# Performance work log

Hardware: AMD Instinct MI355X
Metric: run time of the kernel (lower is better)

The kernel has to match this reference:

```python
import jax, jax.numpy as jnp
import numpy as np

PAD = 4
MAX_DISP = 4


def setup_inputs() -> dict:
    key = jax.random.key(0)
    k1, k2 = jax.random.split(key)
    in1 = jax.random.normal(k1, (8, 256, 128, 128), dtype=jnp.float32)
    in2 = jax.random.normal(k2, (8, 256, 128, 128), dtype=jnp.float32)
    return {"in1": in1, "in2": in2}


def reference(in1, in2):
    # in1, in2: [B, C, H, W]
    H, W = in1.shape[2], in1.shape[3]
    in2_pad = jnp.pad(in2, ((0, 0), (0, 0), (PAD, PAD), (PAD, PAD)))
    D = 2 * MAX_DISP + 1  # 9 displacements per axis -> 81 output channels
    outs = []
    # torch.meshgrid('ij') + zip(offsetx, offsety): dy is the outer (slow) index,
    # dx the inner (fast) index.
    for dy in range(D):
        for dx in range(D):
            # mean over channel dim of elementwise product with shifted window
            corr = jnp.mean(in1 * in2_pad[:, :, dy:dy + H, dx:dx + W],
                            axis=1, keepdims=True)  # [B,1,H,W]
            outs.append(corr)
    return jnp.concatenate(outs, axis=1)  # [B, D*D, H, W]
```

## Files before the change

kernel.cpp:

```cpp
#include <hip/hip_runtime.h>
#include <stdint.h>


#define B_  8
#define C_  256
#define H_  128
#define W_  128
#define ND  9
#define TY  8
#define TW  16
#define KC  32
#define KB  4
#define RR  16
#define JJ  24
#define NITEM 3
#define NDMA  6
#define CS   (H_ * W_)
#define NCH  (C_ / KC)
#define SBUF (KC * RR * JJ)
#define FBUF (KB * RR * JJ * 8)
#define FOFF (2 * SBUF * 4)
#define LDS_TOTAL (FOFF + 2 * FBUF * 2)

typedef short v8s __attribute__((ext_vector_type(8)));
typedef float v4f __attribute__((ext_vector_type(4)));

__device__ __forceinline__ unsigned short f2bf(float f) {
    union { float f; unsigned u; } v; v.f = f;
    return (unsigned short)((v.u + 0x7FFFu + ((v.u >> 16) & 1u)) >> 16);
}

__device__ __forceinline__ void dma16(const float* g, void* lds) {
    __builtin_amdgcn_global_load_lds(
        (const __attribute__((address_space(1))) void*)g,
        (__attribute__((address_space(3))) void*)lds, 16, 0, 0);
}

#define FENCE()        asm volatile("" ::: "memory")
#define WAITV14_BAR()  asm volatile("s_waitcnt vmcnt(14)\n\ts_barrier" ::: "memory")
#define WAITV0_BAR()   asm volatile("s_waitcnt vmcnt(0)\n\ts_barrier" ::: "memory")
#define LGKM0_BAR()    asm volatile("s_waitcnt lgkmcnt(0)\n\ts_barrier" ::: "memory")
#define LGKM0()        asm volatile("s_waitcnt lgkmcnt(0)" ::: "memory")

__global__ __launch_bounds__(512, 2)
void corr_mfma_kernel(const float* __restrict__ in1,
                      const float* __restrict__ in2,
                      float* __restrict__ out) {
    extern __shared__ __align__(16) char ldsbase[];
    float* S = (float*)ldsbase;
    short* F = (short*)(ldsbase + FOFF);

    const int tid  = threadIdx.x;
    const int lane = tid & 63;
    const int w    = tid >> 6;

    const int lin = blockIdx.x;
    const int b   = lin & 7;
    const int idx = lin >> 3;
    const int by  = idx & 15;
    const int bx  = idx >> 4;
    const int x0  = bx * TW;
    const int y0  = by * TY;

    const int i_px = lane & 15;
    const int kb   = lane >> 4;

    const float* dsrc[NDMA];
    int ddst[NDMA];
    #pragma unroll
    for (int t = 0; t < NDMA; ++t) {
        const int q  = w * NDMA + t;
        const int g  = q * 64 + lane;
        const int cc = g / 96;
        const int rm = g % 96;
        const int r  = rm / 6;
        const int jg = rm % 6;
        int gy = y0 - 4 + r;
        int gx = x0 - 4 + jg * 4;
        gy = gy < 0 ? 0 : (gy > H_ - 1 ? H_ - 1 : gy);
        gx = gx < 0 ? 0 : (gx > W_ - 4 ? W_ - 4 : gx);
        dsrc[t] = in2 + ((long)(b * C_ + cc) * H_ + gy) * W_ + gx;
        ddst[t] = q * 1024;
    }

    int soff[NITEM], foff[NITEM];
    bool valid[NITEM];
    #pragma unroll
    for (int it = 0; it < NITEM; ++it) {
        const int s   = tid + it * 512;
        const int ikb = s / (RR * JJ);
        const int ir  = (s / JJ) % RR;
        const int ij  = s % JJ;
        soff[it]  = ikb * 8 * (RR * JJ) + ir * JJ + ij;
        foff[it]  = s * 8;
        valid[it] = ((unsigned)(y0 - 4 + ir) < (unsigned)H_) &&
                    ((unsigned)(x0 - 4 + ij) < (unsigned)W_);
    }

    const float* p1 =
        in1 + (((long)b * C_ + kb * 8) * H_ + (y0 + w)) * W_ + x0 + i_px;

    v4f acc0[ND];
    v4f acc1[5];
    #pragma unroll
    for (int d = 0; d < ND; ++d) acc0[d] = (v4f)0.0f;
    #pragma unroll
    for (int p = 0; p < 5; ++p)  acc1[p] = (v4f)0.0f;

    float a_buf[2][8];
    v8s afrag, afrag_nxt;

    #pragma unroll
    for (int t = 0; t < NDMA; ++t) dma16(dsrc[t], (char*)S + ddst[t]);
    #pragma unroll
    for (int e = 0; e < 8; ++e) a_buf[0][e] = p1[(long)e * CS];
    FENCE();
    #pragma unroll
    for (int t = 0; t < NDMA; ++t)
        dma16(dsrc[t] + (long)KC * CS, (char*)S + SBUF * 4 + ddst[t]);
    #pragma unroll
    for (int e = 0; e < 8; ++e) a_buf[1][e] = p1[(long)KC * CS + (long)e * CS];
    FENCE();
    WAITV14_BAR();
    #pragma unroll
    for (int e = 0; e < 8; ++e) afrag[e] = (short)f2bf(a_buf[0][e]);
    {
        v8s pk[NITEM];
        #pragma unroll
        for (int it = 0; it < NITEM; ++it) {
            #pragma unroll
            for (int e = 0; e < 8; ++e)
                pk[it][e] = (short)f2bf(S[soff[it] + e * (RR * JJ)]);
            if (!valid[it]) pk[it] = (v8s)0;
        }
        #pragma unroll
        for (int it = 0; it < NITEM; ++it)
            *(v8s*)&F[foff[it]] = pk[it];
    }
    LGKM0_BAR();

    #pragma unroll
    for (int k = 0; k < NCH; ++k) {
        const int cb = k & 1;

        if (k + 2 < NCH) {
            const long co = (long)(k + 2) * KC * CS;
            #pragma unroll
            for (int t = 0; t < NDMA; ++t)
                dma16(dsrc[t] + co, (char*)S + cb * (SBUF * 4) + ddst[t]);
            #pragma unroll
            for (int e = 0; e < 8; ++e) a_buf[cb][e] = p1[co + (long)e * CS];
            FENCE();
        }

        #pragma unroll
        for (int dy = 0; dy < ND; ++dy) {
            const int r = w + dy;
            const v8s bf = *(const v8s*)&F[cb * FBUF + ((kb * RR + r) * JJ + i_px) * 8];
            acc0[dy] = __builtin_amdgcn_mfma_f32_16x16x32_bf16(afrag, bf, acc0[dy], 0, 0, 0);
        }
        #pragma unroll
        for (int P = 0; P < 5; ++P) {
            int r = w + 2 * P + (i_px >> 3);
            if (r > RR - 1) r = RR - 1;
            const int j = 16 + (i_px & 7);
            const v8s bf = *(const v8s*)&F[cb * FBUF + ((kb * RR + r) * JJ + j) * 8];
            acc1[P] = __builtin_amdgcn_mfma_f32_16x16x32_bf16(afrag, bf, acc1[P], 0, 0, 0);
        }

        if (k + 1 < NCH) {
            if (k + 2 < NCH) { WAITV14_BAR(); } else { WAITV0_BAR(); }

            #pragma unroll
            for (int e = 0; e < 8; ++e) afrag_nxt[e] = (short)f2bf(a_buf[cb ^ 1][e]);
            v8s pk[NITEM];
            #pragma unroll
            for (int it = 0; it < NITEM; ++it) {
                #pragma unroll
                for (int e = 0; e < 8; ++e)
                    pk[it][e] = (short)f2bf(S[(cb ^ 1) * SBUF + soff[it] + e * (RR * JJ)]);
                if (!valid[it]) pk[it] = (v8s)0;
            }
            #pragma unroll
            for (int it = 0; it < NITEM; ++it)
                *(v8s*)&F[(cb ^ 1) * FBUF + foff[it]] = pk[it];
            afrag = afrag_nxt;

            LGKM0_BAR();
        }
    }

    LGKM0_BAR();
    float* epw = (float*)F + w * (16 * 24);
    const int g = lane >> 4;

    for (int dy = 0; dy < ND; ++dy) {
        #pragma unroll
        for (int q = 0; q < 4; ++q)
            epw[(g * 4 + q) * 24 + i_px] = acc0[dy][q];
        if ((i_px >> 3) == (dy & 1)) {
            #pragma unroll
            for (int q = 0; q < 4; ++q)
                epw[(g * 4 + q) * 24 + 16 + (i_px & 7)] = acc1[dy >> 1][q];
        }
        LGKM0();
        #pragma unroll
        for (int rep = 0; rep < 3; ++rep) {
            const int dx = g + rep * 4;
            if (dx < 9) {
                const float v = epw[i_px * 24 + i_px + dx] * (1.0f / 256.0f);
                out[((((long)b * 81) + dy * 9 + dx) * H_ + (y0 + w)) * W_ + x0 + i_px] = v;
            }
        }
        LGKM0();
    }
}

extern "C" void kernel_launch(void* const* d_in, const int* in_sizes, int n_in,
                              void* d_out, int out_size, void* d_ws, size_t ws_size,
                              hipStream_t stream) {
    const float* in1 = (const float*)d_in[0];
    const float* in2 = (const float*)d_in[1];
    float* outp      = (float*)d_out;
    (void)hipFuncSetAttribute((const void*)corr_mfma_kernel,
                              hipFuncAttributeMaxDynamicSharedMemorySize,
                              LDS_TOTAL);
    corr_mfma_kernel<<<1024, 512, LDS_TOTAL, stream>>>(in1, in2, outp);
}
```

Baseline: 96.02 us.

## Make blocks persistent over four row tiles with cross-tile prefetch

Each block now walks four vertically stacked 8-row tiles instead of one, and the grid shrinks from 1024 to 256 blocks. The first channel chunks of the next tile are prefetched during the last chunks of the current tile, so the pipeline fill and drain is paid once per block rather than once per tile. The epilogue moves to a separate LDS region so it does not conflict with the prefetched buffers. The cost is fewer blocks (256 across the CUs, so less occupancy and parallelism) and more LDS per block.

```diff
diff --git a/kernel.cpp b/kernel.cpp
--- a/kernel.cpp
+++ b/kernel.cpp
@@ -9,6 +9,7 @@
 #define ND  9
 #define TY  8
 #define TW  16
+#define NT  4
 #define KC  32
 #define KB  4
 #define RR  16
@@ -16,11 +17,12 @@
 #define NITEM 3
 #define NDMA  6
 #define CS   (H_ * W_)
-#define NCH  (C_ / KC)
+#define NCH  8
 #define SBUF (KC * RR * JJ)
 #define FBUF (KB * RR * JJ * 8)
 #define FOFF (2 * SBUF * 4)
-#define LDS_TOTAL (FOFF + 2 * FBUF * 2)
+#define EPOFF (FOFF + 2 * FBUF * 2)
+#define LDS_TOTAL (EPOFF + 8 * 16 * JJ * 4)
 
 typedef short v8s __attribute__((ext_vector_type(8)));
 typedef float v4f __attribute__((ext_vector_type(4)));
@@ -47,8 +49,9 @@
                       const float* __restrict__ in2,
                       float* __restrict__ out) {
     extern __shared__ __align__(16) char ldsbase[];
-    float* S = (float*)ldsbase;
-    short* F = (short*)(ldsbase + FOFF);
+    float* S  = (float*)ldsbase;
+    short* F  = (short*)(ldsbase + FOFF);
+    float* EP = (float*)(ldsbase + EPOFF);
 
     const int tid  = threadIdx.x;
     const int lane = tid & 63;
@@ -57,16 +60,14 @@
     const int lin = blockIdx.x;
     const int b   = lin & 7;
     const int idx = lin >> 3;
-    const int by  = idx & 15;
-    const int bx  = idx >> 4;
-    const int x0  = bx * TW;
-    const int y0  = by * TY;
+    const int x0  = (idx & 7) * TW;
+    int y0        = (idx >> 3) * (NT * TY);
 
     const int i_px = lane & 15;
     const int kb   = lane >> 4;
 
-    const float* dsrc[NDMA];
-    int ddst[NDMA];
+    const float* dbase[NDMA];
+    int drr[NDMA], ddst[NDMA];
     #pragma unroll
     for (int t = 0; t < NDMA; ++t) {
         const int q  = w * NDMA + t;
@@ -75,16 +76,22 @@
         const int rm = g % 96;
         const int r  = rm / 6;
         const int jg = rm % 6;
-        int gy = y0 - 4 + r;
         int gx = x0 - 4 + jg * 4;
+        gx = gx < 0 ? 0 : (gx > W_ - 4 ? W_ - 4 : gx);
+        dbase[t] = in2 + (long)(b * C_ + cc) * CS + gx;
+        drr[t]   = r;
+        ddst[t]  = q * 1024;
+    }
+    const float* dsrc[NDMA];
+    #pragma unroll
+    for (int t = 0; t < NDMA; ++t) {
+        int gy = y0 - 4 + drr[t];
         gy = gy < 0 ? 0 : (gy > H_ - 1 ? H_ - 1 : gy);
-        gx = gx < 0 ? 0 : (gx > W_ - 4 ? W_ - 4 : gx);
-        dsrc[t] = in2 + ((long)(b * C_ + cc) * H_ + gy) * W_ + gx;
-        ddst[t] = q * 1024;
-    }
-
-    int soff[NITEM], foff[NITEM];
-    bool valid[NITEM];
+        dsrc[t] = dbase[t] + (long)gy * W_;
+    }
+
+    int soff[NITEM], foff2[NITEM], irr[NITEM];
+    bool vx[NITEM];
     #pragma unroll
     for (int it = 0; it < NITEM; ++it) {
         const int s   = tid + it * 512;
@@ -92,21 +99,16 @@
         const int ir  = (s / JJ) % RR;
         const int ij  = s % JJ;
         soff[it]  = ikb * 8 * (RR * JJ) + ir * JJ + ij;
-        foff[it]  = s * 8;
-        valid[it] = ((unsigned)(y0 - 4 + ir) < (unsigned)H_) &&
-                    ((unsigned)(x0 - 4 + ij) < (unsigned)W_);
+        foff2[it] = s * 8;
+        irr[it]   = ir;
+        vx[it]    = (unsigned)(x0 - 4 + ij) < (unsigned)W_;
     }
 
     const float* p1 =
-        in1 + (((long)b * C_ + kb * 8) * H_ + (y0 + w)) * W_ + x0 + i_px;
+        in1 + ((long)b * C_ + kb * 8) * CS + (long)(y0 + w) * W_ + x0 + i_px;
 
     v4f acc0[ND];
     v4f acc1[5];
-    #pragma unroll
-    for (int d = 0; d < ND; ++d) acc0[d] = (v4f)0.0f;
-    #pragma unroll
-    for (int p = 0; p < 5; ++p)  acc1[p] = (v4f)0.0f;
-
     float a_buf[2][8];
     v8s afrag, afrag_nxt;
 
@@ -125,94 +127,126 @@
     #pragma unroll
     for (int e = 0; e < 8; ++e) afrag[e] = (short)f2bf(a_buf[0][e]);
     {
+        const int y04 = y0 - 4;
         v8s pk[NITEM];
         #pragma unroll
         for (int it = 0; it < NITEM; ++it) {
             #pragma unroll
             for (int e = 0; e < 8; ++e)
                 pk[it][e] = (short)f2bf(S[soff[it] + e * (RR * JJ)]);
-            if (!valid[it]) pk[it] = (v8s)0;
+            if (!(vx[it] && (unsigned)(y04 + irr[it]) < (unsigned)H_)) pk[it] = (v8s)0;
         }
         #pragma unroll
         for (int it = 0; it < NITEM; ++it)
-            *(v8s*)&F[foff[it]] = pk[it];
+            *(v8s*)&F[foff2[it]] = pk[it];
     }
     LGKM0_BAR();
 
-    #pragma unroll
-    for (int k = 0; k < NCH; ++k) {
-        const int cb = k & 1;
-
-        if (k + 2 < NCH) {
-            const long co = (long)(k + 2) * KC * CS;
+    #pragma unroll 1
+    for (int tt = 0; tt < NT; ++tt) {
+        #pragma unroll
+        for (int d = 0; d < ND; ++d) acc0[d] = (v4f)0.0f;
+        #pragma unroll
+        for (int p = 0; p < 5; ++p)  acc1[p] = (v4f)0.0f;
+
+        #pragma unroll
+        for (int k = 0; k < NCH; ++k) {
+            const int cb = k & 1;
+            const bool last_tile  = (tt == NT - 1);
+            const bool has_issue  = (k < 6) || !last_tile;
+            const bool last_chunk = last_tile && (k == 7);
+
+            if (k == 6 && !last_tile) {
+                #pragma unroll
+                for (int t = 0; t < NDMA; ++t) {
+                    int gy = y0 + TY - 4 + drr[t];
+                    gy = gy < 0 ? 0 : (gy > H_ - 1 ? H_ - 1 : gy);
+                    dsrc[t] = dbase[t] + (long)gy * W_;
+                }
+            }
+            if (k < 6) {
+                const long co = (long)(k + 2) * KC * CS;
+                #pragma unroll
+                for (int t = 0; t < NDMA; ++t)
+                    dma16(dsrc[t] + co, (char*)S + cb * (SBUF * 4) + ddst[t]);
+                #pragma unroll
+                for (int e = 0; e < 8; ++e) a_buf[cb][e] = p1[co + (long)e * CS];
+                FENCE();
+            } else if (!last_tile) {
+                const long co = (long)(k - 6) * KC * CS;
+                const float* p1n = p1 + TY * W_;
+                #pragma unroll
+                for (int t = 0; t < NDMA; ++t)
+                    dma16(dsrc[t] + co, (char*)S + cb * (SBUF * 4) + ddst[t]);
+                #pragma unroll
+                for (int e = 0; e < 8; ++e) a_buf[cb][e] = p1n[co + (long)e * CS];
+                FENCE();
+            }
+
             #pragma unroll
-            for (int t = 0; t < NDMA; ++t)
-                dma16(dsrc[t] + co, (char*)S + cb * (SBUF * 4) + ddst[t]);
+            for (int dy = 0; dy < ND; ++dy) {
+                const int r = w + dy;
+                const v8s bf = *(const v8s*)&F[cb * FBUF + ((kb * RR + r) * JJ + i_px) * 8];
+                acc0[dy] = __builtin_amdgcn_mfma_f32_16x16x32_bf16(afrag, bf, acc0[dy], 0, 0, 0);
+            }
             #pragma unroll
-            for (int e = 0; e < 8; ++e) a_buf[cb][e] = p1[co + (long)e * CS];
-            FENCE();
+            for (int P = 0; P < 5; ++P) {
+                int r = w + 2 * P + (i_px >> 3);
+                if (r > RR - 1) r = RR - 1;
+                const int j = 16 + (i_px & 7);
+                const v8s bf = *(const v8s*)&F[cb * FBUF + ((kb * RR + r) * JJ + j) * 8];
+                acc1[P] = __builtin_amdgcn_mfma_f32_16x16x32_bf16(afrag, bf, acc1[P], 0, 0, 0);
+            }
+
+            if (!last_chunk) {
+                if (has_issue) { WAITV14_BAR(); } else { WAITV0_BAR(); }
+
+                #pragma unroll
+                for (int e = 0; e < 8; ++e) afrag_nxt[e] = (short)f2bf(a_buf[cb ^ 1][e]);
+                const int y04 = y0 + ((k == 7) ? TY : 0) - 4;
+                v8s pk[NITEM];
+                #pragma unroll
+                for (int it = 0; it < NITEM; ++it) {
+                    #pragma unroll
+                    for (int e = 0; e < 8; ++e)
+                        pk[it][e] = (short)f2bf(S[(cb ^ 1) * SBUF + soff[it] + e * (RR * JJ)]);
+                    if (!(vx[it] && (unsigned)(y04 + irr[it]) < (unsigned)H_)) pk[it] = (v8s)0;
+                }
+                #pragma unroll
+                for (int it = 0; it < NITEM; ++it)
+                    *(v8s*)&F[(cb ^ 1) * FBUF + foff2[it]] = pk[it];
+                afrag = afrag_nxt;
+
+                LGKM0_BAR();
+            }
+
+            if (k == 7) {
+                float* epw = EP + w * (16 * JJ);
+                const int g = lane >> 4;
+                for (int dy = 0; dy < ND; ++dy) {
+                    #pragma unroll
+                    for (int q = 0; q < 4; ++q)
+                        epw[(g * 4 + q) * JJ + i_px] = acc0[dy][q];
+                    if ((i_px >> 3) == (dy & 1)) {
+                        #pragma unroll
+                        for (int q = 0; q < 4; ++q)
+                            epw[(g * 4 + q) * JJ + 16 + (i_px & 7)] = acc1[dy >> 1][q];
+                    }
+                    LGKM0();
+                    #pragma unroll
+                    for (int rep = 0; rep < 3; ++rep) {
+                        const int dx = g + rep * 4;
+                        if (dx < 9) {
+                            const float v = epw[i_px * JJ + i_px + dx] * (1.0f / 256.0f);
+                            out[((((long)b * 81) + dy * 9 + dx) * H_ + (y0 + w)) * W_ + x0 + i_px] = v;
+                        }
+                    }
+                    LGKM0();
+                }
+            }
         }
-
-        #pragma unroll
-        for (int dy = 0; dy < ND; ++dy) {
-            const int r = w + dy;
-            const v8s bf = *(const v8s*)&F[cb * FBUF + ((kb * RR + r) * JJ + i_px) * 8];
-            acc0[dy] = __builtin_amdgcn_mfma_f32_16x16x32_bf16(afrag, bf, acc0[dy], 0, 0, 0);
-        }
-        #pragma unroll
-        for (int P = 0; P < 5; ++P) {
-            int r = w + 2 * P + (i_px >> 3);
-            if (r > RR - 1) r = RR - 1;
-            const int j = 16 + (i_px & 7);
-            const v8s bf = *(const v8s*)&F[cb * FBUF + ((kb * RR + r) * JJ + j) * 8];
-            acc1[P] = __builtin_amdgcn_mfma_f32_16x16x32_bf16(afrag, bf, acc1[P], 0, 0, 0);
-        }
-
-        if (k + 1 < NCH) {
-            if (k + 2 < NCH) { WAITV14_BAR(); } else { WAITV0_BAR(); }
-
-            #pragma unroll
-            for (int e = 0; e < 8; ++e) afrag_nxt[e] = (short)f2bf(a_buf[cb ^ 1][e]);
-            v8s pk[NITEM];
-            #pragma unroll
-            for (int it = 0; it < NITEM; ++it) {
-                #pragma unroll
-                for (int e = 0; e < 8; ++e)
-                    pk[it][e] = (short)f2bf(S[(cb ^ 1) * SBUF + soff[it] + e * (RR * JJ)]);
-                if (!valid[it]) pk[it] = (v8s)0;
-            }
-            #pragma unroll
-            for (int it = 0; it < NITEM; ++it)
-                *(v8s*)&F[(cb ^ 1) * FBUF + foff[it]] = pk[it];
-            afrag = afrag_nxt;
-
-            LGKM0_BAR();
-        }
-    }
-
-    LGKM0_BAR();
-    float* epw = (float*)F + w * (16 * 24);
-    const int g = lane >> 4;
-
-    for (int dy = 0; dy < ND; ++dy) {
-        #pragma unroll
-        for (int q = 0; q < 4; ++q)
-            epw[(g * 4 + q) * 24 + i_px] = acc0[dy][q];
-        if ((i_px >> 3) == (dy & 1)) {
-            #pragma unroll
-            for (int q = 0; q < 4; ++q)
-                epw[(g * 4 + q) * 24 + 16 + (i_px & 7)] = acc1[dy >> 1][q];
-        }
-        LGKM0();
-        #pragma unroll
-        for (int rep = 0; rep < 3; ++rep) {
-            const int dx = g + rep * 4;
-            if (dx < 9) {
-                const float v = epw[i_px * 24 + i_px + dx] * (1.0f / 256.0f);
-                out[((((long)b * 81) + dy * 9 + dx) * H_ + (y0 + w)) * W_ + x0 + i_px] = v;
-            }
-        }
-        LGKM0();
+        y0 += TY;
+        p1 += TY * W_;
     }
 }
 
@@ -225,5 +259,5 @@
     (void)hipFuncSetAttribute((const void*)corr_mfma_kernel,
                               hipFuncAttributeMaxDynamicSharedMemorySize,
                               LDS_TOTAL);
-    corr_mfma_kernel<<<1024, 512, LDS_TOTAL, stream>>>(in1, in2, outp);
-}
+    corr_mfma_kernel<<<256, 512, LDS_TOTAL, stream>>>(in1, in2, outp);
+}
```

Result: no change. 97.09 us (+1.1%).
